# Kernel optimization log

Measured on AMD Instinct MI355X. Metric: run time of the kernel, lower is better.

The kernel has to match this reference:

```python
import jax, jax.numpy as jnp
import jax.lax as lax
import numpy as np

X_NUM = 512
Y_NUM = 512
GRID = 1.0 / 512.0
MIN_X = 0.0
MIN_Y = 0.0
N_POINTS = 400000
BATCH = 4
NUM_CLASSES = 20


def setup_inputs():
    key = jax.random.key(0)
    ks = jax.random.split(key, 32)
    # rows 0/1: x,y coords in [0,1) so they land inside the 512x512 grid; rows 2-5: features
    xy = jax.random.uniform(ks[0], (2, N_POINTS), jnp.float32, 0.0, 1.0 - 1e-6)
    feat = jax.random.normal(ks[1], (4, N_POINTS), jnp.float32) * 0.5
    points = jnp.concatenate([xy, feat], 0)
    batch_ids = jax.random.randint(ks[2], (N_POINTS,), 0, BATCH, jnp.int32)
    inp = {"batch_ids": batch_ids, "points": points, "batch_size": BATCH}

    def lin(k, o, i):
        return jax.random.normal(k, (o, i), jnp.float32) * (1.0 / np.sqrt(i))

    ki = 3
    # pointwise conv1d stacks: (name, out_ch, in_ch)
    for name, o, i in [("0", 16, 6), ("1", 16, 16), ("v0", 16, 18), ("v1", 16, 32), ("2", 32, 32)]:
        inp["w" + name] = lin(ks[ki], o, i); ki += 1
        inp["b" + name] = jnp.zeros((o,), jnp.float32)
        inp["s" + name] = jax.random.uniform(ks[ki], (o,), jnp.float32, 0.5, 1.5); ki += 1
        inp["t" + name] = jax.random.normal(ks[ki], (o,), jnp.float32) * 0.1; ki += 1
    inp["w2d"] = jax.random.normal(ks[ki], (4, 32, 32, 3, 3), jnp.float32) * (1.0 / np.sqrt(32 * 9)); ki += 1
    inp["b2d"] = jnp.zeros((4, 32), jnp.float32)
    inp["s2d"] = jax.random.uniform(ks[ki], (4, 32), jnp.float32, 0.5, 1.5); ki += 1
    inp["t2d"] = jax.random.normal(ks[ki], (4, 32), jnp.float32) * 0.1; ki += 1
    inp["w3"] = lin(ks[ki], NUM_CLASSES, 64); ki += 1
    inp["b3"] = jnp.zeros((NUM_CLASSES,), jnp.float32)
    return inp


def _pconv(x, w, b, s, t):
    # 1x1 conv1d + BatchNorm(inference affine) + ReLU; x: [Cin, N]
    return jax.nn.relu((w @ x + b[:, None]) * s[:, None] + t[:, None])


def _scatter_max(v, gids, n):
    # v: [C, N] -> [C, n]; empty segments filled with 0 (torch_scatter fill_value=0,
    # and all scattered values here are post-ReLU >= 0)
    seg = jax.ops.segment_max(v.T, gids, num_segments=n).T
    return jnp.where(jnp.isneginf(seg), 0.0, seg)


def _bilinear(img, ix, iy):
    # grid_sample(align_corners=False, padding zeros) in pixel coords; img: [C, H, W]
    C, H, W = img.shape
    x0 = jnp.floor(ix); y0 = jnp.floor(iy)
    wx = ix - x0; wy = iy - y0
    x0i = x0.astype(jnp.int32); y0i = y0.astype(jnp.int32)

    def tap(yi, xi):
        valid = ((yi >= 0) & (yi < H) & (xi >= 0) & (xi < W)).astype(img.dtype)
        return img[:, jnp.clip(yi, 0, H - 1), jnp.clip(xi, 0, W - 1)] * valid

    return (tap(y0i, x0i) * (1 - wx) * (1 - wy) + tap(y0i, x0i + 1) * wx * (1 - wy)
            + tap(y0i + 1, x0i) * (1 - wx) * wy + tap(y0i + 1, x0i + 1) * wx * wy)


def _forward(batch_ids, points, batch_size, w0, b0, s0, t0, w1, b1, s1, t1,
             wv0, bv0, sv0, tv0, wv1, bv1, sv1, tv1, w2, b2, s2, t2,
             w2d, b2d, s2d, t2d, w3, b3):
    x_g = jnp.floor((points[0] - MIN_X) / GRID).astype(jnp.int32)
    y_g = jnp.floor((points[1] - MIN_Y) / GRID).astype(jnp.int32)
    gids = batch_ids.astype(jnp.int32) * (X_NUM * Y_NUM) + y_g * X_NUM + x_g
    grid_num = batch_size * Y_NUM * X_NUM

    h = _pconv(points, w0, b0, s0, t0)       # [16, N]
    h = _pconv(h, w1, b1, s1, t1)            # [16, N]
    vx = (x_g.astype(jnp.float32) + 0.5) * GRID + MIN_X
    vy = (y_g.astype(jnp.float32) + 0.5) * GRID + MIN_Y
    h = jnp.concatenate([h, (points[0] - vx)[None], (points[1] - vy)[None]], 0)  # [18, N]

    # VFE blocks: pointwise conv -> scatter_max over voxel ids -> gather back -> concat
    o = _pconv(h, wv0, bv0, sv0, tv0)        # [16, N]
    h = jnp.concatenate([o, _scatter_max(o, gids, grid_num)[:, gids]], 0)  # [32, N]
    o = _pconv(h, wv1, bv1, sv1, tv1)        # [16, N]
    h = jnp.concatenate([o, _scatter_max(o, gids, grid_num)[:, gids]], 0)  # [32, N]

    point0 = _pconv(h, w2, b2, s2, t2)       # [32, N]
    grid = _scatter_max(point0, gids, grid_num)
    grid = grid.reshape(32, batch_size, Y_NUM, X_NUM).transpose(1, 0, 2, 3)  # [B,32,Y,X]

    for i in range(4):
        p = 1 if i == 0 else 2
        grid = lax.conv_general_dilated(grid, w2d[i], (1, 1), ((p, p), (p, p)),
                                        rhs_dilation=(p, p),
                                        dimension_numbers=("NCHW", "OIHW", "NCHW"))
        grid = jax.nn.relu((grid + b2d[i][None, :, None, None]) * s2d[i][None, :, None, None]
                           + t2d[i][None, :, None, None])

    # interpolate (grid_sample) back to points; pixel coords reduce to (x-MIN)/GRID - 1
    img = grid.transpose(1, 0, 2, 3).reshape(32, batch_size * Y_NUM, X_NUM)
    ix = (points[0] - MIN_X) / GRID - 1.0
    iy = (points[1] - MIN_Y) / GRID - 1.0 + batch_ids.astype(jnp.float32) * Y_NUM
    point1 = _bilinear(img, ix, iy)          # [32, N]

    point = jnp.concatenate([point0, point1], 0)  # [64, N]
    return w3 @ point + b3[:, None]               # [num_classes, N]


def reference(batch_ids, points, batch_size, w0, b0, s0, t0, w1, b1, s1, t1,
              wv0, bv0, sv0, tv0, wv1, bv1, sv1, tv1, w2, b2, s2, t2,
              w2d, b2d, s2d, t2d, w3, b3):
    return _forward(batch_ids, points, batch_size, w0, b0, s0, t0, w1, b1, s1, t1,
                    wv0, bv0, sv0, tv0, wv1, bv1, sv1, tv1, w2, b2, s2, t2,
                    w2d, b2d, s2d, t2d, w3, b3)
```

## Files before the change

### kernel.cpp

```cpp
#include <hip/hip_runtime.h>
#include <hip/hip_bf16.h>
#include <hip/hip_fp16.h>

#define N_PTS 400000
#define XN 512
#define YN 512
#define BATCHN 4
#define VOX (XN*YN)
#define GRID_NUM (BATCHN*VOX)

typedef unsigned long long u64;
typedef __attribute__((ext_vector_type(8))) _Float16 f16x8;
typedef __attribute__((ext_vector_type(4))) float f32x4;

static __device__ __forceinline__ float relu_(float x){ return fmaxf(x, 0.0f); }
static __device__ __forceinline__ int voxel_id(float px, float py, int b){
    int xg = (int)floorf(px*512.0f);
    int yg = (int)floorf(py*512.0f);
    return b*VOX + yg*XN + xg;
}

static __device__ __forceinline__ u64 packh4(const float* v){
    u64 r = 0;
    #pragma unroll
    for (int j=0;j<4;j++){
        unsigned short h = __half_as_ushort(__float2half_rn(v[j]));
        r |= (u64)h << (16*j);
    }
    return r;
}
static __device__ __forceinline__ void unpackh4(u64 w, float* o){
    #pragma unroll
    for (int j=0;j<4;j++)
        o[j] = __half2float(__ushort_as_half((unsigned short)(w >> (16*j))));
}
static __device__ __forceinline__ u64 pkmax4(u64 a, u64 b){
    u64 r = 0;
    #pragma unroll
    for (int j=0;j<4;j++){
        u64 x = (a >> (16*j)) & 0xFFFFull;
        u64 y = (b >> (16*j)) & 0xFFFFull;
        r |= (x > y ? x : y) << (16*j);
    }
    return r;
}

__global__ void kZero(float4* __restrict__ p, int n4){
    int i = blockIdx.x*256 + threadIdx.x;
    const float4 z = make_float4(0.f,0.f,0.f,0.f);
    for (; i < n4; i += gridDim.x*256) p[i] = z;
}

__global__ void kDiag(float* __restrict__ o, int n, float v){
    int i = blockIdx.x*256 + threadIdx.x;
    for (; i < n; i += gridDim.x*256) o[i] = v;
}

__global__ void kHist(const int* __restrict__ bid, const float* __restrict__ pts,
                      unsigned* __restrict__ offs, int* __restrict__ gids)
{
    int i = blockIdx.x*256 + threadIdx.x;
    if (i >= N_PTS) return;
    int gid = voxel_id(pts[i], pts[N_PTS+i], bid[i]);
    gids[i] = gid;
    atomicAdd(&offs[gid], 1u);
}

__global__ void kScan1(unsigned* __restrict__ offs, unsigned* __restrict__ partials)
{
    __shared__ unsigned sa[256], sb[256];
    const int t = threadIdx.x;
    const int g = blockIdx.x*256 + t;
    unsigned v = offs[g];
    sa[t] = v;
    __syncthreads();
    unsigned* src = sa; unsigned* dst = sb;
    #pragma unroll
    for (int d=1; d<256; d<<=1){
        dst[t] = src[t] + ((t>=d) ? src[t-d] : 0u);
        __syncthreads();
        unsigned* tmp = src; src = dst; dst = tmp;
    }
    unsigned incl = src[t];
    offs[g] = incl - v;
    if (t == 255) partials[blockIdx.x] = incl;
}
__global__ void kScan2(unsigned* __restrict__ partials)
{
    __shared__ unsigned sa[256], sb[256];
    const int t = threadIdx.x;
    unsigned loc[16]; unsigned sum = 0;
    #pragma unroll
    for (int j=0;j<16;j++){ loc[j] = partials[t*16+j]; sum += loc[j]; }
    sa[t] = sum;
    __syncthreads();
    unsigned* src = sa; unsigned* dst = sb;
    #pragma unroll
    for (int d=1; d<256; d<<=1){
        dst[t] = src[t] + ((t>=d) ? src[t-d] : 0u);
        __syncthreads();
        unsigned* tmp = src; src = dst; dst = tmp;
    }
    unsigned run = src[t] - sum;
    #pragma unroll
    for (int j=0;j<16;j++){ unsigned c = loc[j]; partials[t*16+j] = run; run += c; }
}
__global__ void kScan3(unsigned* __restrict__ offs, const unsigned* __restrict__ partials)
{
    int g = blockIdx.x*256 + threadIdx.x;
    offs[g] += partials[blockIdx.x];
}

__global__ void kA(const int* __restrict__ bid, const float* __restrict__ pts,
                   const int* __restrict__ gids,
                   const float* __restrict__ w0, const float* __restrict__ b0,
                   const float* __restrict__ s0, const float* __restrict__ t0,
                   const float* __restrict__ w1, const float* __restrict__ b1,
                   const float* __restrict__ s1, const float* __restrict__ t1,
                   const float* __restrict__ wv0, const float* __restrict__ bv0,
                   const float* __restrict__ sv0, const float* __restrict__ tv0,
                   u64* __restrict__ obufA,
                   unsigned* __restrict__ offs, unsigned* __restrict__ order)
{
    int i = blockIdx.x*256 + threadIdx.x;
    if (i >= N_PTS) return;
    float p[6];
    #pragma unroll
    for (int r=0;r<6;r++) p[r] = pts[r*N_PTS+i];
    int xg = (int)floorf(p[0]*512.0f);
    int yg = (int)floorf(p[1]*512.0f);

    float h0[16];
    #pragma unroll
    for (int o=0;o<16;o++){
        float a = b0[o];
        #pragma unroll
        for (int k=0;k<6;k++) a = fmaf(w0[o*6+k], p[k], a);
        h0[o] = relu_(fmaf(a, s0[o], t0[o]));
    }
    float h1[16];
    #pragma unroll
    for (int o=0;o<16;o++){
        float a = b1[o];
        #pragma unroll
        for (int k=0;k<16;k++) a = fmaf(w1[o*16+k], h0[k], a);
        h1[o] = relu_(fmaf(a, s1[o], t1[o]));
    }
    float dx = p[0] - ((float)xg + 0.5f)*(1.0f/512.0f);
    float dy = p[1] - ((float)yg + 0.5f)*(1.0f/512.0f);
    float vv[16];
    #pragma unroll
    for (int o=0;o<16;o++){
        float a = bv0[o];
        #pragma unroll
        for (int k=0;k<16;k++) a = fmaf(wv0[o*18+k], h1[k], a);
        a = fmaf(wv0[o*18+16], dx, a);
        a = fmaf(wv0[o*18+17], dy, a);
        vv[o] = relu_(fmaf(a, sv0[o], tv0[o]));
    }
    u64* op = obufA + (size_t)i*4;
    #pragma unroll
    for (int q=0;q<4;q++) op[q] = packh4(&vv[q*4]);

    int gid = gids[i];
    unsigned pos = atomicAdd(&offs[gid], 1u);
    order[pos] = (unsigned)i;
}

__global__ void kSegMax(const unsigned* __restrict__ offs, const unsigned* __restrict__ order,
                        const u64* __restrict__ src, u64* __restrict__ dst)
{
    int v = blockIdx.x*256 + threadIdx.x;
    unsigned s = v ? offs[v-1] : 0u;
    unsigned e = offs[v];
    if (e <= s) return;
    u64 m0=0,m1=0,m2=0,m3=0;
    for (unsigned p=s; p<e; ++p){
        const u64* q = src + (size_t)order[p]*4;
        m0 = pkmax4(m0, q[0]); m1 = pkmax4(m1, q[1]);
        m2 = pkmax4(m2, q[2]); m3 = pkmax4(m3, q[3]);
    }
    u64* d = dst + (size_t)v*4;
    d[0]=m0; d[1]=m1; d[2]=m2; d[3]=m3;
}

__global__ void kGridMax(const unsigned* __restrict__ offs, const unsigned* __restrict__ order,
                         const u64* __restrict__ src, u64* __restrict__ dst)
{
    int v = blockIdx.x*256 + threadIdx.x;
    unsigned s = v ? offs[v-1] : 0u;
    unsigned e = offs[v];
    u64 m[8];
    #pragma unroll
    for (int q=0;q<8;q++) m[q] = 0ull;
    for (unsigned p=s; p<e; ++p){
        const u64* q = src + (size_t)order[p]*8;
        #pragma unroll
        for (int j=0;j<8;j++) m[j] = pkmax4(m[j], q[j]);
    }
    u64* d = dst + (size_t)v*8;
    #pragma unroll
    for (int q=0;q<8;q++) d[q] = m[q];
}

__global__ void kB(const int* __restrict__ gids,
                   const float* __restrict__ w, const float* __restrict__ bb,
                   const float* __restrict__ ss, const float* __restrict__ tt,
                   const u64* __restrict__ obufA, const u64* __restrict__ seg0,
                   u64* __restrict__ obufB)
{
    int i = blockIdx.x*256 + threadIdx.x;
    if (i >= N_PTS) return;
    int gid = gids[i];
    float h[32];
    const u64* ap = obufA + (size_t)i*4;
    #pragma unroll
    for (int q=0;q<4;q++) unpackh4(ap[q], &h[q*4]);
    const u64* sp = seg0 + (size_t)gid*4;
    #pragma unroll
    for (int q=0;q<4;q++) unpackh4(sp[q], &h[16+q*4]);

    float o[16];
    #pragma unroll
    for (int c=0;c<16;c++){
        float a = bb[c];
        #pragma unroll
        for (int k=0;k<32;k++) a = fmaf(w[c*32+k], h[k], a);
        o[c] = relu_(fmaf(a, ss[c], tt[c]));
    }
    u64* op = obufB + (size_t)i*4;
    #pragma unroll
    for (int q=0;q<4;q++) op[q] = packh4(&o[q*4]);
}

__global__ void kC(const int* __restrict__ gids,
                   const float* __restrict__ w, const float* __restrict__ bb,
                   const float* __restrict__ ss, const float* __restrict__ tt,
                   const float* __restrict__ w3,
                   const u64* __restrict__ obufB, const u64* __restrict__ seg1,
                   u64* __restrict__ pbuf, float* __restrict__ outp)
{
    int i = blockIdx.x*256 + threadIdx.x;
    if (i >= N_PTS) return;
    int gid = gids[i];
    float h[32];
    const u64* ap = obufB + (size_t)i*4;
    #pragma unroll
    for (int q=0;q<4;q++) unpackh4(ap[q], &h[q*4]);
    const u64* sp = seg1 + (size_t)gid*4;
    #pragma unroll
    for (int q=0;q<4;q++) unpackh4(sp[q], &h[16+q*4]);

    float p0v[32];
    #pragma unroll
    for (int c=0;c<32;c++){
        float a = bb[c];
        #pragma unroll
        for (int k=0;k<32;k++) a = fmaf(w[c*32+k], h[k], a);
        p0v[c] = relu_(fmaf(a, ss[c], tt[c]));
    }
    u64* pp = pbuf + (size_t)i*8;
    #pragma unroll
    for (int q=0;q<8;q++) pp[q] = packh4(&p0v[q*4]);
    #pragma unroll
    for (int k=0;k<20;k++){
        float a = 0.f;
        #pragma unroll
        for (int c=0;c<32;c++) a = fmaf(w3[k*64+c], p0v[c], a);
        outp[(size_t)k*N_PTS+i] = a;
    }
}

template<int P>
__global__ __launch_bounds__(256,2) void convM(
    const _Float16* __restrict__ in, _Float16* __restrict__ out,
    const float* __restrict__ W32, const float* __restrict__ bb,
    const float* __restrict__ ss, const float* __restrict__ tt)
{
    constexpr int TW = 32, TH = 16;
    constexpr int TIW = TW + 2*P, TIH = TH + 2*P;
    __shared__ uint4 sA[TIH*TIW*5];
    __shared__ uint4 sW4[9*2*64];
    const int tid = threadIdx.x;
    const int lane = tid & 63, wv = tid >> 6;
    const int x0 = blockIdx.x*TW, y0 = blockIdx.y*TH, bz = blockIdx.z;
    const _Float16* inB = in + (size_t)bz*VOX*32;

    {
        _Float16* sWh = (_Float16*)sW4;
        for (int idx = tid; idx < 9216; idx += 256){
            int j = idx & 7, ln = (idx>>3) & 63, rest = idx >> 9;
            int t = rest >> 1, nt = rest & 1;
            int ic = (ln>>4)*8 + j, oc = nt*16 + (ln&15);
            sWh[idx] = (_Float16)W32[((size_t)oc*32 + ic)*9 + t];
        }
    }
    for (int u = tid; u < TIH*TIW*4; u += 256){
        int g = u & 3;
        int pxr = u >> 2;
        int px = pxr % TIW, r = pxr / TIW;
        int gy = y0 - P + r, gx = x0 - P + px;
        uint4 v = make_uint4(0,0,0,0);
        if ((unsigned)gy < 512u && (unsigned)gx < 512u)
            v = *(const uint4*)(inB + (((size_t)gy*512 + gx)*32 + g*8));
        sA[(r*TIW + px)*5 + g] = v;
    }
    __syncthreads();

    const f16x8* pA = (const f16x8*)sA;
    const f16x8* pW = (const f16x8*)sW4;
    const int aoff = (lane&15)*5 + (lane>>4);
    const int rowbase = wv*4;

    f32x4 acc[8][2];
    #pragma unroll
    for (int m=0;m<8;m++){ acc[m][0]=(f32x4)0.f; acc[m][1]=(f32x4)0.f; }

    #pragma unroll
    for (int t=0;t<9;t++){
        const int ky = t/3, kx = t%3;
        f16x8 b0 = pW[(t*2+0)*64 + lane];
        f16x8 b1 = pW[(t*2+1)*64 + lane];
        #pragma unroll
        for (int m=0;m<8;m++){
            int r = rowbase + (m>>1) + ky*P;
            int pxb = (m&1)*16 + kx*P;
            f16x8 a = pA[(r*TIW + pxb)*5 + aoff];
            acc[m][0] = __builtin_amdgcn_mfma_f32_16x16x32_f16(a, b0, acc[m][0], 0,0,0);
            acc[m][1] = __builtin_amdgcn_mfma_f32_16x16x32_f16(a, b1, acc[m][1], 0,0,0);
        }
    }

    float bn[2], sn[2], tn[2];
    #pragma unroll
    for (int n=0;n<2;n++){
        int oc = n*16 + (lane&15);
        bn[n] = bb[oc]; sn[n] = ss[oc]; tn[n] = tt[oc];
    }
    _Float16* outB = out + (size_t)bz*VOX*32;
    #pragma unroll
    for (int m=0;m<8;m++){
        int y = y0 + rowbase + (m>>1);
        int xb = x0 + (m&1)*16 + (lane>>4)*4;
        #pragma unroll
        for (int n=0;n<2;n++){
            int oc = n*16 + (lane&15);
            #pragma unroll
            for (int r=0;r<4;r++){
                float v = relu_(fmaf(acc[m][n][r] + bn[n], sn[n], tn[n]));
                outB[(((size_t)y*512) + (xb + r))*32 + oc] = (_Float16)v;
            }
        }
    }
}

__global__ void kFinal(const int* __restrict__ bid, const float* __restrict__ pts,
                       const _Float16* __restrict__ gridH,
                       const float* __restrict__ w3, const float* __restrict__ b3,
                       float* __restrict__ outp)
{
    int i = blockIdx.x*256 + threadIdx.x;
    if (i >= N_PTS) return;
    float px = pts[i], py = pts[N_PTS+i];
    int b = bid[i];
    float ix = px*512.0f - 1.0f;
    float iy = py*512.0f - 1.0f + (float)(b*512);
    float x0f = floorf(ix), y0f = floorf(iy);
    float wx = ix - x0f, wy = iy - y0f;
    int x0 = (int)x0f, y0 = (int)y0f;

    float p1[32];
    #pragma unroll
    for (int c=0;c<32;c++) p1[c] = 0.f;
    #pragma unroll
    for (int t=0;t<4;t++){
        int yi = y0 + (t>>1);
        int xi = x0 + (t&1);
        if (yi < 0 || yi >= BATCHN*YN || xi < 0 || xi >= XN) continue;
        float wgt = ((t>>1)? wy : 1.0f-wy) * ((t&1)? wx : 1.0f-wx);
        const uint4* tp = (const uint4*)(gridH + ((size_t)yi*XN + xi)*32);
        #pragma unroll
        for (int q=0;q<4;q++){
            uint4 v = tp[q];
            const unsigned int* vu = (const unsigned int*)&v;
            #pragma unroll
            for (int e=0;e<4;e++){
                float lo = __half2float(__ushort_as_half((unsigned short)(vu[e] & 0xFFFF)));
                float hi = __half2float(__ushort_as_half((unsigned short)(vu[e] >> 16)));
                p1[q*8 + e*2 + 0] = fmaf(wgt, lo, p1[q*8 + e*2 + 0]);
                p1[q*8 + e*2 + 1] = fmaf(wgt, hi, p1[q*8 + e*2 + 1]);
            }
        }
    }

    #pragma unroll
    for (int k=0;k<20;k++){
        float a = outp[(size_t)k*N_PTS + i] + b3[k];
        #pragma unroll
        for (int c=0;c<32;c++) a = fmaf(w3[k*64+32+c], p1[c], a);
        outp[(size_t)k*N_PTS + i] = a;
    }
}

extern "C" void kernel_launch(void* const* d_in, const int* in_sizes, int n_in,
                              void* d_out, int out_size, void* d_ws, size_t ws_size,
                              hipStream_t stream)
{
    const int*   bid = (const int*)  d_in[0];
    const float* pts = (const float*)d_in[1];
    const float* w0  = (const float*)d_in[3];
    const float* b0  = (const float*)d_in[4];
    const float* s0  = (const float*)d_in[5];
    const float* t0  = (const float*)d_in[6];
    const float* w1  = (const float*)d_in[7];
    const float* b1  = (const float*)d_in[8];
    const float* s1  = (const float*)d_in[9];
    const float* t1  = (const float*)d_in[10];
    const float* wv0 = (const float*)d_in[11];
    const float* bv0 = (const float*)d_in[12];
    const float* sv0 = (const float*)d_in[13];
    const float* tv0 = (const float*)d_in[14];
    const float* wv1 = (const float*)d_in[15];
    const float* bv1 = (const float*)d_in[16];
    const float* sv1 = (const float*)d_in[17];
    const float* tv1 = (const float*)d_in[18];
    const float* w2  = (const float*)d_in[19];
    const float* b2  = (const float*)d_in[20];
    const float* s2  = (const float*)d_in[21];
    const float* t2  = (const float*)d_in[22];
    const float* w2d = (const float*)d_in[23];
    const float* b2d = (const float*)d_in[24];
    const float* s2d = (const float*)d_in[25];
    const float* t2d = (const float*)d_in[26];
    const float* w3  = (const float*)d_in[27];
    const float* b3  = (const float*)d_in[28];

    const size_t MB = 1024*1024;
    const size_t NEED = 192*MB;
    if (ws_size < NEED){
        kDiag<<<512,256,0,stream>>>((float*)d_out, out_size, (float)(ws_size>>20));
        return;
    }

    char* ws = (char*)d_ws;
    u64*      gridV    = (u64*)ws;
    _Float16* ping     = (_Float16*)ws;
    _Float16* pong     = (_Float16*)(ws + 64*MB);
    u64*      seg0     = (u64*)(ws + 64*MB);
    u64*      seg1     = (u64*)(ws + 96*MB);
    unsigned* offs     = (unsigned*)(ws + 128*MB);
    unsigned* partials = (unsigned*)(ws + 132*MB);
    unsigned* order    = (unsigned*)(ws + 133*MB);
    int*      gids     = (int*)(ws + 135*MB);
    u64*      obufA    = (u64*)(ws + 137*MB);
    u64*      obufB    = (u64*)(ws + 150*MB);
    u64*      pbuf     = (u64*)(ws + 163*MB);

    kZero<<<256,256,0,stream>>>((float4*)offs, (int)(GRID_NUM*4/16));

    const int nb = (N_PTS + 255)/256;
    const int nv = GRID_NUM/256;

    kHist <<<nb,256,0,stream>>>(bid, pts, offs, gids);
    kScan1<<<nv,256,0,stream>>>(offs, partials);
    kScan2<<<1,256,0,stream>>>(partials);
    kScan3<<<nv,256,0,stream>>>(offs, partials);

    kA<<<nb,256,0,stream>>>(bid, pts, gids, w0,b0,s0,t0, w1,b1,s1,t1,
                            wv0,bv0,sv0,tv0, obufA, offs, order);
    kSegMax<<<nv,256,0,stream>>>(offs, order, obufA, seg0);
    kB<<<nb,256,0,stream>>>(gids, wv1,bv1,sv1,tv1, obufA, seg0, obufB);
    kSegMax<<<nv,256,0,stream>>>(offs, order, obufB, seg1);
    kC<<<nb,256,0,stream>>>(gids, w2,b2,s2,t2, w3, obufB, seg1, pbuf, (float*)d_out);
    kGridMax<<<nv,256,0,stream>>>(offs, order, pbuf, gridV);

    dim3 cgrid(XN/32, YN/16, BATCHN);
    convM<1><<<cgrid,256,0,stream>>>(ping, pong, w2d + 0*9216, b2d + 0,  s2d + 0,  t2d + 0);
    convM<2><<<cgrid,256,0,stream>>>(pong, ping, w2d + 1*9216, b2d + 32, s2d + 32, t2d + 32);
    convM<2><<<cgrid,256,0,stream>>>(ping, pong, w2d + 2*9216, b2d + 64, s2d + 64, t2d + 64);
    convM<2><<<cgrid,256,0,stream>>>(pong, ping, w2d + 3*9216, b2d + 96, s2d + 96, t2d + 96);

    kFinal<<<nb,256,0,stream>>>(bid, pts, ping, w3, b3, (float*)d_out);
}
```

Before: 423.4 us.

## Read conv input tiles directly from global memory instead of LDS staging

The 3x3 dilated conv kernel no longer stages the haloed input tile in shared memory. Each MFMA A-fragment is now loaded straight from global memory, with a separate edge variant that clamps addresses and zeros out-of-bounds lanes. This drops the LDS fill loop and its footprint, so occupancy is raised to 4 blocks per SM. The cost is nine redundant global/L2 reads per input element, with each 16-byte load sitting directly in front of an MFMA.

```diff
diff --git a/kernel.cpp b/kernel.cpp
--- a/kernel.cpp
+++ b/kernel.cpp
@@ -271,15 +271,43 @@
     }
 }
 
+template<int P, bool EDGE>
+static __device__ __forceinline__ void conv_core(
+    const _Float16* __restrict__ inB, const f16x8* __restrict__ pW,
+    int y0, int x0, int rowbase, int lane, f32x4 acc[8][2])
+{
+    const int lx = lane & 15, chunk = (lane >> 4) * 8;
+    #pragma unroll
+    for (int t=0;t<9;t++){
+        const int ky = t/3, kx = t%3;
+        f16x8 b0 = pW[(t*2+0)*64 + lane];
+        f16x8 b1 = pW[(t*2+1)*64 + lane];
+        #pragma unroll
+        for (int m=0;m<8;m++){
+            int gy = y0 + rowbase + (m>>1) + ky*P - P;
+            int gx = x0 + (m&1)*16 + kx*P - P + lx;
+            f16x8 a;
+            if (EDGE){
+                bool v = ((unsigned)gy < 512u) && ((unsigned)gx < 512u);
+                int cy = v ? gy : 0, cx = v ? gx : 0;
+                a = *(const f16x8*)(inB + ((size_t)cy*512 + cx)*32 + chunk);
+                if (!v) a = (f16x8)(_Float16)0.0f;
+            } else {
+                a = *(const f16x8*)(inB + ((size_t)gy*512 + gx)*32 + chunk);
+            }
+            acc[m][0] = __builtin_amdgcn_mfma_f32_16x16x32_f16(a, b0, acc[m][0], 0,0,0);
+            acc[m][1] = __builtin_amdgcn_mfma_f32_16x16x32_f16(a, b1, acc[m][1], 0,0,0);
+        }
+    }
+}
+
 template<int P>
-__global__ __launch_bounds__(256,2) void convM(
+__global__ __launch_bounds__(256,4) void convM(
     const _Float16* __restrict__ in, _Float16* __restrict__ out,
     const float* __restrict__ W32, const float* __restrict__ bb,
     const float* __restrict__ ss, const float* __restrict__ tt)
 {
     constexpr int TW = 32, TH = 16;
-    constexpr int TIW = TW + 2*P, TIH = TH + 2*P;
-    __shared__ uint4 sA[TIH*TIW*5];
     __shared__ uint4 sW4[9*2*64];
     const int tid = threadIdx.x;
     const int lane = tid & 63, wv = tid >> 6;
@@ -295,41 +323,18 @@
             sWh[idx] = (_Float16)W32[((size_t)oc*32 + ic)*9 + t];
         }
     }
-    for (int u = tid; u < TIH*TIW*4; u += 256){
-        int g = u & 3;
-        int pxr = u >> 2;
-        int px = pxr % TIW, r = pxr / TIW;
-        int gy = y0 - P + r, gx = x0 - P + px;
-        uint4 v = make_uint4(0,0,0,0);
-        if ((unsigned)gy < 512u && (unsigned)gx < 512u)
-            v = *(const uint4*)(inB + (((size_t)gy*512 + gx)*32 + g*8));
-        sA[(r*TIW + px)*5 + g] = v;
-    }
     __syncthreads();
 
-    const f16x8* pA = (const f16x8*)sA;
     const f16x8* pW = (const f16x8*)sW4;
-    const int aoff = (lane&15)*5 + (lane>>4);
     const int rowbase = wv*4;
 
     f32x4 acc[8][2];
     #pragma unroll
     for (int m=0;m<8;m++){ acc[m][0]=(f32x4)0.f; acc[m][1]=(f32x4)0.f; }
 
-    #pragma unroll
-    for (int t=0;t<9;t++){
-        const int ky = t/3, kx = t%3;
-        f16x8 b0 = pW[(t*2+0)*64 + lane];
-        f16x8 b1 = pW[(t*2+1)*64 + lane];
-        #pragma unroll
-        for (int m=0;m<8;m++){
-            int r = rowbase + (m>>1) + ky*P;
-            int pxb = (m&1)*16 + kx*P;
-            f16x8 a = pA[(r*TIW + pxb)*5 + aoff];
-            acc[m][0] = __builtin_amdgcn_mfma_f32_16x16x32_f16(a, b0, acc[m][0], 0,0,0);
-            acc[m][1] = __builtin_amdgcn_mfma_f32_16x16x32_f16(a, b1, acc[m][1], 0,0,0);
-        }
-    }
+    const bool interior = (x0 >= P) && (x0 + TW + P <= XN) && (y0 >= P) && (y0 + TH + P <= YN);
+    if (interior) conv_core<P,false>(inB, pW, y0, x0, rowbase, lane, acc);
+    else          conv_core<P,true >(inB, pW, y0, x0, rowbase, lane, acc);
 
     float bn[2], sn[2], tn[2];
     #pragma unroll
```

Result: slower. 745.9 us (+76.2%).
